# Performance work log

Hardware: AMD Instinct MI355X
Metric: run time of the kernel (lower is better)

## Reference

```python
import jax, jax.numpy as jnp
import numpy as np

N = 8192   # n_vertex
F = 1      # input_dim
H = 32     # hidden_dim
K = 2      # k_order -> hops 0..K (3 taps)
B = 2
T = 24
E = 16 * N # edges


def _sym_renorm_adj(src, dst, n):
    # A from COO ones, add self loops, D^{-1/2} (A+I) D^{-1/2}
    A = np.zeros((n, n), dtype=np.float32)
    np.add.at(A, (src, dst), 1.0)
    A += np.eye(n, dtype=np.float32)
    dinv = 1.0 / np.sqrt(A.sum(axis=1))
    return (dinv[:, None] * A * dinv[None, :]).astype(np.float32)


def setup_inputs() -> dict:
    key = jax.random.key(0)
    ks = jax.random.split(key, 16)
    rng = np.random.default_rng(0)
    src = rng.integers(0, N, size=E)
    dst = rng.integers(0, N, size=E)
    edge_index = jnp.asarray(np.stack([src, dst]).astype(np.int64))
    gso = jnp.asarray(_sym_renorm_adj(src, dst, N))
    Cin = (K + 1) * (F + H)  # stacked hop features of [x, h]
    s = 0.02
    p = lambda k, shp: (jax.random.normal(k, shp, dtype=jnp.float32) * s)
    inp = {
        "x": jax.random.normal(ks[0], (B, T, N, F), dtype=jnp.float32),
        "edge_index": edge_index,
        "gso": gso,
        "enc_Wr": p(ks[1], (Cin, H)), "enc_br": jnp.zeros((H,), jnp.float32),
        "enc_Wu": p(ks[2], (Cin, H)), "enc_bu": jnp.zeros((H,), jnp.float32),
        "enc_Wc": p(ks[3], (Cin, H)), "enc_bc": jnp.zeros((H,), jnp.float32),
        "dec_Wr": p(ks[4], (Cin, H)), "dec_br": jnp.zeros((H,), jnp.float32),
        "dec_Wu": p(ks[5], (Cin, H)), "dec_bu": jnp.zeros((H,), jnp.float32),
        "dec_Wc": p(ks[6], (Cin, H)), "dec_bc": jnp.zeros((H,), jnp.float32),
        "po_W1": p(ks[7], (H, H)), "po_b1": jnp.zeros((H,), jnp.float32),
        "po_W2": p(ks[8], (H, F)), "po_b2": jnp.zeros((F,), jnp.float32),
    }
    return inp


def _gconv(inp, gso, W, b):
    x0 = inp
    x1 = jnp.einsum("nm,bmc->bnc", gso, x0)
    x2 = jnp.einsum("nm,bmc->bnc", gso, x1)
    xs = jnp.concatenate([x0, x1, x2], axis=-1)
    return xs @ W + b


def _cell(xin, h, gso, Wr, br, Wu, bu, Wc, bc):
    # DCGRU cell: gates from K-hop graph conv of [x, h]
    xh = jnp.concatenate([xin, h], axis=-1)
    r = jax.nn.sigmoid(_gconv(xh, gso, Wr, br))
    u = jax.nn.sigmoid(_gconv(xh, gso, Wu, bu))
    c = jnp.tanh(_gconv(jnp.concatenate([xin, r * h], axis=-1), gso, Wc, bc))
    return u * h + (1.0 - u) * c


def reference(x, edge_index, gso,
              enc_Wr, enc_br, enc_Wu, enc_bu, enc_Wc, enc_bc,
              dec_Wr, dec_br, dec_Wu, dec_bu, dec_Wc, dec_bc,
              po_W1, po_b1, po_W2, po_b2):
    del edge_index  # GSO already built from it (no_grad in original)
    b, t, n, f = x.shape
    h0 = jnp.zeros((b, n, H), x.dtype)

    def enc_step(h, xt):
        return _cell(xt, h, gso, enc_Wr, enc_br, enc_Wu, enc_bu, enc_Wc, enc_bc), None

    h, _ = jax.lax.scan(enc_step, h0, jnp.transpose(x, (1, 0, 2, 3)))

    prev0 = jnp.zeros((b, n, f), x.dtype)

    def dec_step(carry, _):
        hh, prev = carry
        hh = _cell(prev, hh, gso, dec_Wr, dec_br, dec_Wu, dec_bu, dec_Wc, dec_bc)
        z = jax.nn.relu(hh @ po_W1 + po_b1)  # dropout is identity in eval
        pred = z @ po_W2 + po_b2
        return (hh, pred), pred

    _, preds = jax.lax.scan(dec_step, (h, prev0), None, length=t)
    return jnp.transpose(preds, (1, 0, 2, 3))  # (B,T,N,F)
```

## Files before the change

kernel.cpp:

```cpp
#include <hip/hip_runtime.h>


#define NV  8192
#define TT  24
#define BB  2
#define CC  33
#define JJ  66
#define HD  32
#define CAP 64
#define NPB 8

__global__ __launch_bounds__(256) void build_ell(const float* __restrict__ gso,
                                                 int* __restrict__ ellc,
                                                 float* __restrict__ ellv,
                                                 int* __restrict__ rcnt) {
    int gtid = blockIdx.x * 256 + threadIdx.x;
    int row  = gtid >> 6;
    int lane = threadIdx.x & 63;
    if (row >= NV) return;
    const float* r = gso + (size_t)row * NV;
    int cnt = 0;
    const int base = row * CAP;
    for (int c0 = 0; c0 < NV; c0 += 256) {
        const float4 v = *reinterpret_cast<const float4*>(r + c0 + lane * 4);
        const float vv[4] = {v.x, v.y, v.z, v.w};
#pragma unroll
        for (int q = 0; q < 4; ++q) {
            unsigned long long m = __ballot(vv[q] != 0.0f);
            if (vv[q] != 0.0f) {
                int pos = cnt + __popcll(m & ((1ull << lane) - 1ull));
                if (pos < CAP) {
                    ellc[base + pos] = c0 + lane * 4 + q;
                    ellv[base + pos] = vv[q];
                }
            }
            cnt += __popcll(m);
        }
    }
    if (lane == 0) rcnt[row] = cnt < CAP ? cnt : CAP;
}

__global__ __launch_bounds__(256) void init_xh(const float* __restrict__ x,
                                               float* __restrict__ XH) {
    int idx = blockIdx.x * 256 + threadIdx.x;
    if (idx >= NV * JJ) return;
    int n = idx / JJ;
    int j = idx - n * JJ;
    int b = j / CC, c = j - b * CC;
    float v = 0.f;
    if (c == 0) v = x[((size_t)b * TT + 0) * NV + n];
    XH[idx] = v;
}

__global__ __launch_bounds__(256) void spmm1(const int* __restrict__ ellc,
                                             const float* __restrict__ ellv,
                                             const int* __restrict__ rcnt,
                                             const float* __restrict__ Xin,
                                             float* __restrict__ Xout) {
    int idx = blockIdx.x * 256 + threadIdx.x;
    if (idx >= NV * 33) return;
    int n  = idx / 33;
    int j2 = idx - n * 33;
    int cnt  = rcnt[n];
    int base = n * CAP;
    float2 acc = {0.f, 0.f};
    for (int k = 0; k < cnt; ++k) {
        float s = ellv[base + k];
        const float2 xv = *reinterpret_cast<const float2*>(
            Xin + (size_t)ellc[base + k] * JJ + 2 * j2);
        acc.x = fmaf(s, xv.x, acc.x);
        acc.y = fmaf(s, xv.y, acc.y);
    }
    *reinterpret_cast<float2*>(Xout + (size_t)n * JJ + 2 * j2) = acc;
}

__global__ __launch_bounds__(256) void hop2_gates(const int* __restrict__ ellc,
                                                  const float* __restrict__ ellv,
                                                  const int* __restrict__ rcnt,
                                                  const float* __restrict__ XH,
                                                  const float* __restrict__ X1,
                                                  const float* __restrict__ Wr,
                                                  const float* __restrict__ br,
                                                  const float* __restrict__ Wu,
                                                  const float* __restrict__ bu,
                                                  float* __restrict__ U,
                                                  float* __restrict__ XC) {
    __shared__ float x2s[NPB][JJ];
    int n0 = blockIdx.x * NPB;
    for (int e = threadIdx.x; e < NPB * 33; e += 256) {
        int ln = e / 33;
        int j2 = e - ln * 33;
        int n  = n0 + ln;
        int cnt  = rcnt[n];
        int base = n * CAP;
        float2 acc = {0.f, 0.f};
        for (int k = 0; k < cnt; ++k) {
            float s = ellv[base + k];
            const float2 xv = *reinterpret_cast<const float2*>(
                X1 + (size_t)ellc[base + k] * JJ + 2 * j2);
            acc.x = fmaf(s, xv.x, acc.x);
            acc.y = fmaf(s, xv.y, acc.y);
        }
        x2s[ln][2 * j2]     = acc.x;
        x2s[ln][2 * j2 + 1] = acc.y;
    }
    __syncthreads();
    for (int e = threadIdx.x; e < NPB * BB * HD; e += 256) {
        int j  = e & 31;
        int p  = e >> 5;
        int ln = p >> 1;
        int b  = p & 1;
        int n  = n0 + ln;
        const float* xh = XH + (size_t)n * JJ + b * CC;
        const float* x1 = X1 + (size_t)n * JJ + b * CC;
        const float* x2 = &x2s[ln][b * CC];
        float accr = br[j], accu = bu[j];
#pragma unroll
        for (int i = 0; i < CC; ++i) {
            accr = fmaf(xh[i], Wr[i * HD + j], accr);
            accu = fmaf(xh[i], Wu[i * HD + j], accu);
        }
#pragma unroll
        for (int i = 0; i < CC; ++i) {
            accr = fmaf(x1[i], Wr[(CC + i) * HD + j], accr);
            accu = fmaf(x1[i], Wu[(CC + i) * HD + j], accu);
        }
#pragma unroll
        for (int i = 0; i < CC; ++i) {
            accr = fmaf(x2[i], Wr[(2 * CC + i) * HD + j], accr);
            accu = fmaf(x2[i], Wu[(2 * CC + i) * HD + j], accu);
        }
        float rg = 1.f / (1.f + expf(-accr));
        float ug = 1.f / (1.f + expf(-accu));
        U[(size_t)n * 64 + b * HD + j] = ug;
        float h = xh[1 + j];
        XC[(size_t)n * JJ + b * CC + 1 + j] = rg * h;
        if (j == 0) XC[(size_t)n * JJ + b * CC] = xh[0];
    }
}

__global__ __launch_bounds__(256) void hop2_cand(const int* __restrict__ ellc,
                                                 const float* __restrict__ ellv,
                                                 const int* __restrict__ rcnt,
                                                 const float* __restrict__ XC,
                                                 const float* __restrict__ Y1,
                                                 const float* __restrict__ Wc,
                                                 const float* __restrict__ bc,
                                                 const float* __restrict__ U,
                                                 float* __restrict__ XH,
                                                 const float* __restrict__ xsrc,
                                                 int mode, int t_next,
                                                 const float* __restrict__ W1,
                                                 const float* __restrict__ b1,
                                                 const float* __restrict__ W2,
                                                 const float* __restrict__ b2,
                                                 float* __restrict__ out,
                                                 int t_out) {
    __shared__ float y2s[NPB][JJ];
    int n0 = blockIdx.x * NPB;
    for (int e = threadIdx.x; e < NPB * 33; e += 256) {
        int ln = e / 33;
        int j2 = e - ln * 33;
        int n  = n0 + ln;
        int cnt  = rcnt[n];
        int base = n * CAP;
        float2 acc = {0.f, 0.f};
        for (int k = 0; k < cnt; ++k) {
            float s = ellv[base + k];
            const float2 xv = *reinterpret_cast<const float2*>(
                Y1 + (size_t)ellc[base + k] * JJ + 2 * j2);
            acc.x = fmaf(s, xv.x, acc.x);
            acc.y = fmaf(s, xv.y, acc.y);
        }
        y2s[ln][2 * j2]     = acc.x;
        y2s[ln][2 * j2 + 1] = acc.y;
    }
    __syncthreads();
    for (int e = threadIdx.x; e < NPB * BB * HD; e += 256) {
        int j  = e & 31;
        int p  = e >> 5;
        int ln = p >> 1;
        int b  = p & 1;
        int n  = n0 + ln;
        const float* xc = XC + (size_t)n * JJ + b * CC;
        const float* y1 = Y1 + (size_t)n * JJ + b * CC;
        const float* y2 = &y2s[ln][b * CC];
        float acc = bc[j];
#pragma unroll
        for (int i = 0; i < CC; ++i) acc = fmaf(xc[i], Wc[i * HD + j], acc);
#pragma unroll
        for (int i = 0; i < CC; ++i) acc = fmaf(y1[i], Wc[(CC + i) * HD + j], acc);
#pragma unroll
        for (int i = 0; i < CC; ++i) acc = fmaf(y2[i], Wc[(2 * CC + i) * HD + j], acc);
        float c = tanhf(acc);
        float u = U[(size_t)n * 64 + b * HD + j];
        float* hp = XH + (size_t)n * JJ + b * CC + 1 + j;
        float h = u * (*hp) + (1.f - u) * c;
        *hp = h;
        if (mode == 2) {
            float z = b1[j];
#pragma unroll
            for (int i = 0; i < HD; ++i)
                z = fmaf(__shfl(h, i, 32), W1[i * HD + j], z);
            z = fmaxf(z, 0.f);
            float pz = z * W2[j];
#pragma unroll
            for (int off = 16; off; off >>= 1) pz += __shfl_xor(pz, off, 32);
            if (j == 0) {
                float pred = pz + b2[0];
                out[((size_t)b * TT + t_out) * NV + n] = pred;
                XH[(size_t)n * JJ + b * CC] = pred;
            }
        } else if (j == 0) {
            float xin = (mode == 0) ? xsrc[((size_t)b * TT + t_next) * NV + n] : 0.f;
            XH[(size_t)n * JJ + b * CC] = xin;
        }
    }
}

extern "C" void kernel_launch(void* const* d_in, const int* in_sizes, int n_in,
                              void* d_out, int out_size, void* d_ws, size_t ws_size,
                              hipStream_t stream) {
    const float* x      = (const float*)d_in[0];
    const float* gso    = (const float*)d_in[2];
    const float* enc_Wr = (const float*)d_in[3];
    const float* enc_br = (const float*)d_in[4];
    const float* enc_Wu = (const float*)d_in[5];
    const float* enc_bu = (const float*)d_in[6];
    const float* enc_Wc = (const float*)d_in[7];
    const float* enc_bc = (const float*)d_in[8];
    const float* dec_Wr = (const float*)d_in[9];
    const float* dec_br = (const float*)d_in[10];
    const float* dec_Wu = (const float*)d_in[11];
    const float* dec_bu = (const float*)d_in[12];
    const float* dec_Wc = (const float*)d_in[13];
    const float* dec_bc = (const float*)d_in[14];
    const float* po_W1  = (const float*)d_in[15];
    const float* po_b1  = (const float*)d_in[16];
    const float* po_W2  = (const float*)d_in[17];
    const float* po_b2  = (const float*)d_in[18];
    float* out = (float*)d_out;

    char* p = (char*)d_ws;
    auto alloc = [&](size_t bytes) {
        char* q = p;
        p += (bytes + 255) & ~(size_t)255;
        return q;
    };
    int*   ellc = (int*)  alloc((size_t)NV * CAP * 4);
    float* ellv = (float*)alloc((size_t)NV * CAP * 4);
    int*   rcnt = (int*)  alloc((size_t)NV * 4);
    float* XH   = (float*)alloc((size_t)NV * JJ * 4);
    float* X1   = (float*)alloc((size_t)NV * JJ * 4);
    float* XC   = (float*)alloc((size_t)NV * JJ * 4);
    float* Y1   = (float*)alloc((size_t)NV * JJ * 4);
    float* U    = (float*)alloc((size_t)NV * 64 * 4);

    const dim3 blk(256);
    const dim3 g_build(NV / 4);
    const dim3 g_init((NV * JJ + 255) / 256);
    const dim3 g_feat2((NV * 33 + 255) / 256);
    const dim3 g_node(NV / NPB);

    hipLaunchKernelGGL(build_ell, g_build, blk, 0, stream, gso, ellc, ellv, rcnt);
    hipLaunchKernelGGL(init_xh, g_init, blk, 0, stream, x, XH);

    for (int t = 0; t < TT; ++t) {
        hipLaunchKernelGGL(spmm1, g_feat2, blk, 0, stream, ellc, ellv, rcnt, XH, X1);
        hipLaunchKernelGGL(hop2_gates, g_node, blk, 0, stream, ellc, ellv, rcnt,
                           XH, X1, enc_Wr, enc_br, enc_Wu, enc_bu, U, XC);
        hipLaunchKernelGGL(spmm1, g_feat2, blk, 0, stream, ellc, ellv, rcnt, XC, Y1);
        hipLaunchKernelGGL(hop2_cand, g_node, blk, 0, stream, ellc, ellv, rcnt,
                           XC, Y1, enc_Wc, enc_bc, U, XH,
                           x, (t + 1 < TT) ? 0 : 1, t + 1,
                           po_W1, po_b1, po_W2, po_b2, out, 0);
    }
    for (int t = 0; t < TT; ++t) {
        hipLaunchKernelGGL(spmm1, g_feat2, blk, 0, stream, ellc, ellv, rcnt, XH, X1);
        hipLaunchKernelGGL(hop2_gates, g_node, blk, 0, stream, ellc, ellv, rcnt,
                           XH, X1, dec_Wr, dec_br, dec_Wu, dec_bu, U, XC);
        hipLaunchKernelGGL(spmm1, g_feat2, blk, 0, stream, ellc, ellv, rcnt, XC, Y1);
        hipLaunchKernelGGL(hop2_cand, g_node, blk, 0, stream, ellc, ellv, rcnt,
                           XC, Y1, dec_Wc, dec_bc, U, XH,
                           x, 2, 0,
                           po_W1, po_b1, po_W2, po_b2, out, t);
    }
}
```

Baseline: 6.179 ms.

## Fuse two-hop SpMM into gate kernels via direct neighbor-of-neighbor gather

Drops the separate one-hop SpMM launches. Each gates/candidate kernel now computes both diffusion hops per node by walking neighbors of neighbors, with one 64-lane wavefront per node and shuffles for the dense weight products. The feature layout is also split into a 64-wide hidden array and a 2-wide input array, and state initialisation is folded into the ELL build. This halves launches per timestep and removes the intermediate hop-1 buffers. The price is recomputing hop-1 rows for every neighbor, which multiplies gather traffic by roughly the average degree.

```diff
diff --git a/kernel.cpp b/kernel.cpp
--- a/kernel.cpp
+++ b/kernel.cpp
@@ -3,17 +3,16 @@
 
 #define NV  8192
 #define TT  24
-#define BB  2
-#define CC  33
-#define JJ  66
+#define CAP 64
 #define HD  32
-#define CAP 64
-#define NPB 8
 
 __global__ __launch_bounds__(256) void build_ell(const float* __restrict__ gso,
                                                  int* __restrict__ ellc,
                                                  float* __restrict__ ellv,
-                                                 int* __restrict__ rcnt) {
+                                                 int* __restrict__ rcnt,
+                                                 float* __restrict__ XHh,
+                                                 float* __restrict__ XHx,
+                                                 const float* __restrict__ x) {
     int gtid = blockIdx.x * 256 + threadIdx.x;
     int row  = gtid >> 6;
     int lane = threadIdx.x & 63;
@@ -38,183 +37,131 @@
         }
     }
     if (lane == 0) rcnt[row] = cnt < CAP ? cnt : CAP;
-}
-
-__global__ __launch_bounds__(256) void init_xh(const float* __restrict__ x,
-                                               float* __restrict__ XH) {
-    int idx = blockIdx.x * 256 + threadIdx.x;
-    if (idx >= NV * JJ) return;
-    int n = idx / JJ;
-    int j = idx - n * JJ;
-    int b = j / CC, c = j - b * CC;
-    float v = 0.f;
-    if (c == 0) v = x[((size_t)b * TT + 0) * NV + n];
-    XH[idx] = v;
-}
-
-__global__ __launch_bounds__(256) void spmm1(const int* __restrict__ ellc,
-                                             const float* __restrict__ ellv,
-                                             const int* __restrict__ rcnt,
-                                             const float* __restrict__ Xin,
-                                             float* __restrict__ Xout) {
-    int idx = blockIdx.x * 256 + threadIdx.x;
-    if (idx >= NV * 33) return;
-    int n  = idx / 33;
-    int j2 = idx - n * 33;
-    int cnt  = rcnt[n];
-    int base = n * CAP;
-    float2 acc = {0.f, 0.f};
-    for (int k = 0; k < cnt; ++k) {
-        float s = ellv[base + k];
-        const float2 xv = *reinterpret_cast<const float2*>(
-            Xin + (size_t)ellc[base + k] * JJ + 2 * j2);
-        acc.x = fmaf(s, xv.x, acc.x);
-        acc.y = fmaf(s, xv.y, acc.y);
-    }
-    *reinterpret_cast<float2*>(Xout + (size_t)n * JJ + 2 * j2) = acc;
-}
-
-__global__ __launch_bounds__(256) void hop2_gates(const int* __restrict__ ellc,
-                                                  const float* __restrict__ ellv,
-                                                  const int* __restrict__ rcnt,
-                                                  const float* __restrict__ XH,
-                                                  const float* __restrict__ X1,
-                                                  const float* __restrict__ Wr,
-                                                  const float* __restrict__ br,
-                                                  const float* __restrict__ Wu,
-                                                  const float* __restrict__ bu,
-                                                  float* __restrict__ U,
-                                                  float* __restrict__ XC) {
-    __shared__ float x2s[NPB][JJ];
-    int n0 = blockIdx.x * NPB;
-    for (int e = threadIdx.x; e < NPB * 33; e += 256) {
-        int ln = e / 33;
-        int j2 = e - ln * 33;
-        int n  = n0 + ln;
-        int cnt  = rcnt[n];
-        int base = n * CAP;
-        float2 acc = {0.f, 0.f};
-        for (int k = 0; k < cnt; ++k) {
-            float s = ellv[base + k];
-            const float2 xv = *reinterpret_cast<const float2*>(
-                X1 + (size_t)ellc[base + k] * JJ + 2 * j2);
-            acc.x = fmaf(s, xv.x, acc.x);
-            acc.y = fmaf(s, xv.y, acc.y);
+    XHh[row * 64 + lane] = 0.f;
+    if (lane < 2) XHx[row * 2 + lane] = x[((size_t)lane * TT) * NV + row];
+}
+
+#define GATHER2(Fh, Fx, x1, x1x, x2, x2x)                                   \
+    float x1 = 0.f, x1x = 0.f, x2 = 0.f, x2x = 0.f;                         \
+    for (int k = 0; k < cnt; ++k) {                                         \
+        const int   ck = __shfl(myc, k);                                    \
+        const float vk = __shfl(myv, k);                                    \
+        const int   pc = __shfl(nbc, k);                                    \
+        const int   nc = lane < pc ? ellc[ck * CAP + lane] : 0;             \
+        const float nv = lane < pc ? ellv[ck * CAP + lane] : 0.f;           \
+        float a = 0.f, ax = 0.f;                                            \
+        for (int p = 0; p < pc; ++p) {                                      \
+            const int   c = __shfl(nc, p);                                  \
+            const float v = __shfl(nv, p);                                  \
+            a  = fmaf(v, Fh[c * 64 + lane], a);                             \
+            ax = fmaf(v, Fx[c * 2 + b], ax);                                \
+        }                                                                   \
+        x2 = fmaf(vk, a, x2); x2x = fmaf(vk, ax, x2x);                      \
+        if (ck == n) { x1 = a; x1x = ax; }                                  \
+    }
+
+__global__ __launch_bounds__(512) void gates_k(const int* __restrict__ ellc,
+                                               const float* __restrict__ ellv,
+                                               const int* __restrict__ rcnt,
+                                               const float* __restrict__ XHh,
+                                               const float* __restrict__ XHx,
+                                               const float* __restrict__ Wr,
+                                               const float* __restrict__ br,
+                                               const float* __restrict__ Wu,
+                                               const float* __restrict__ bu,
+                                               float* __restrict__ U,
+                                               float* __restrict__ XCh,
+                                               float* __restrict__ XCx) {
+    const int lane = threadIdx.x & 63;
+    const int j = lane & 31, b = lane >> 5, jb = b << 5;
+    const int n = blockIdx.x * 8 + (threadIdx.x >> 6);
+    const int   cnt = rcnt[n];
+    const int   myc = lane < cnt ? ellc[n * CAP + lane] : 0;
+    const float myv = lane < cnt ? ellv[n * CAP + lane] : 0.f;
+    const int   nbc = lane < cnt ? rcnt[myc] : 0;
+    GATHER2(XHh, XHx, x1, x1x, x2, x2x)
+    const float h  = XHh[n * 64 + lane];
+    const float xh = XHx[n * 2 + b];
+    float accr = br[j], accu = bu[j];
+    accr = fmaf(xh,  Wr[j],           accr);  accu = fmaf(xh,  Wu[j],           accu);
+    accr = fmaf(x1x, Wr[33 * 32 + j], accr);  accu = fmaf(x1x, Wu[33 * 32 + j], accu);
+    accr = fmaf(x2x, Wr[66 * 32 + j], accr);  accu = fmaf(x2x, Wu[66 * 32 + j], accu);
+#pragma unroll
+    for (int m = 0; m < 32; ++m) {
+        const float f0 = __shfl(h,  jb + m);
+        const float f1 = __shfl(x1, jb + m);
+        const float f2 = __shfl(x2, jb + m);
+        accr = fmaf(f0, Wr[(1 + m) * 32 + j],  accr);
+        accu = fmaf(f0, Wu[(1 + m) * 32 + j],  accu);
+        accr = fmaf(f1, Wr[(34 + m) * 32 + j], accr);
+        accu = fmaf(f1, Wu[(34 + m) * 32 + j], accu);
+        accr = fmaf(f2, Wr[(67 + m) * 32 + j], accr);
+        accu = fmaf(f2, Wu[(67 + m) * 32 + j], accu);
+    }
+    const float rg = 1.f / (1.f + expf(-accr));
+    const float ug = 1.f / (1.f + expf(-accu));
+    U[n * 64 + lane]   = ug;
+    XCh[n * 64 + lane] = rg * h;
+    if (j == 0) XCx[n * 2 + b] = xh;
+}
+
+__global__ __launch_bounds__(512) void cand_k(const int* __restrict__ ellc,
+                                              const float* __restrict__ ellv,
+                                              const int* __restrict__ rcnt,
+                                              const float* __restrict__ XCh,
+                                              const float* __restrict__ XCx,
+                                              float* XHh, float* XHx,
+                                              const float* __restrict__ U,
+                                              const float* __restrict__ Wc,
+                                              const float* __restrict__ bc,
+                                              const float* __restrict__ x,
+                                              const float* __restrict__ W1,
+                                              const float* __restrict__ b1,
+                                              const float* __restrict__ W2,
+                                              const float* __restrict__ b2,
+                                              float* __restrict__ out,
+                                              int mode, int t_next, int t_out) {
+    const int lane = threadIdx.x & 63;
+    const int j = lane & 31, b = lane >> 5, jb = b << 5;
+    const int n = blockIdx.x * 8 + (threadIdx.x >> 6);
+    const int   cnt = rcnt[n];
+    const int   myc = lane < cnt ? ellc[n * CAP + lane] : 0;
+    const float myv = lane < cnt ? ellv[n * CAP + lane] : 0.f;
+    const int   nbc = lane < cnt ? rcnt[myc] : 0;
+    GATHER2(XCh, XCx, y1, y1x, y2, y2x)
+    const float h   = XHh[n * 64 + lane];
+    const float xc  = XCx[n * 2 + b];
+    const float xch = XCh[n * 64 + lane];
+    float acc = bc[j];
+    acc = fmaf(xc,  Wc[j],           acc);
+    acc = fmaf(y1x, Wc[33 * 32 + j], acc);
+    acc = fmaf(y2x, Wc[66 * 32 + j], acc);
+#pragma unroll
+    for (int m = 0; m < 32; ++m) {
+        acc = fmaf(__shfl(xch, jb + m), Wc[(1 + m) * 32 + j],  acc);
+        acc = fmaf(__shfl(y1,  jb + m), Wc[(34 + m) * 32 + j], acc);
+        acc = fmaf(__shfl(y2,  jb + m), Wc[(67 + m) * 32 + j], acc);
+    }
+    const float cc = tanhf(acc);
+    const float u  = U[n * 64 + lane];
+    const float hn = u * h + (1.f - u) * cc;
+    XHh[n * 64 + lane] = hn;
+    if (mode == 2) {
+        float z = b1[j];
+#pragma unroll
+        for (int m = 0; m < 32; ++m)
+            z = fmaf(__shfl(hn, jb + m), W1[m * 32 + j], z);
+        float pz = fmaxf(z, 0.f) * W2[j];
+#pragma unroll
+        for (int off = 16; off; off >>= 1) pz += __shfl_xor(pz, off);
+        if (j == 0) {
+            const float pred = pz + b2[0];
+            out[((size_t)b * TT + t_out) * NV + n] = pred;
+            XHx[n * 2 + b] = pred;
         }
-        x2s[ln][2 * j2]     = acc.x;
-        x2s[ln][2 * j2 + 1] = acc.y;
-    }
-    __syncthreads();
-    for (int e = threadIdx.x; e < NPB * BB * HD; e += 256) {
-        int j  = e & 31;
-        int p  = e >> 5;
-        int ln = p >> 1;
-        int b  = p & 1;
-        int n  = n0 + ln;
-        const float* xh = XH + (size_t)n * JJ + b * CC;
-        const float* x1 = X1 + (size_t)n * JJ + b * CC;
-        const float* x2 = &x2s[ln][b * CC];
-        float accr = br[j], accu = bu[j];
-#pragma unroll
-        for (int i = 0; i < CC; ++i) {
-            accr = fmaf(xh[i], Wr[i * HD + j], accr);
-            accu = fmaf(xh[i], Wu[i * HD + j], accu);
-        }
-#pragma unroll
-        for (int i = 0; i < CC; ++i) {
-            accr = fmaf(x1[i], Wr[(CC + i) * HD + j], accr);
-            accu = fmaf(x1[i], Wu[(CC + i) * HD + j], accu);
-        }
-#pragma unroll
-        for (int i = 0; i < CC; ++i) {
-            accr = fmaf(x2[i], Wr[(2 * CC + i) * HD + j], accr);
-            accu = fmaf(x2[i], Wu[(2 * CC + i) * HD + j], accu);
-        }
-        float rg = 1.f / (1.f + expf(-accr));
-        float ug = 1.f / (1.f + expf(-accu));
-        U[(size_t)n * 64 + b * HD + j] = ug;
-        float h = xh[1 + j];
-        XC[(size_t)n * JJ + b * CC + 1 + j] = rg * h;
-        if (j == 0) XC[(size_t)n * JJ + b * CC] = xh[0];
-    }
-}
-
-__global__ __launch_bounds__(256) void hop2_cand(const int* __restrict__ ellc,
-                                                 const float* __restrict__ ellv,
-                                                 const int* __restrict__ rcnt,
-                                                 const float* __restrict__ XC,
-                                                 const float* __restrict__ Y1,
-                                                 const float* __restrict__ Wc,
-                                                 const float* __restrict__ bc,
-                                                 const float* __restrict__ U,
-                                                 float* __restrict__ XH,
-                                                 const float* __restrict__ xsrc,
-                                                 int mode, int t_next,
-                                                 const float* __restrict__ W1,
-                                                 const float* __restrict__ b1,
-                                                 const float* __restrict__ W2,
-                                                 const float* __restrict__ b2,
-                                                 float* __restrict__ out,
-                                                 int t_out) {
-    __shared__ float y2s[NPB][JJ];
-    int n0 = blockIdx.x * NPB;
-    for (int e = threadIdx.x; e < NPB * 33; e += 256) {
-        int ln = e / 33;
-        int j2 = e - ln * 33;
-        int n  = n0 + ln;
-        int cnt  = rcnt[n];
-        int base = n * CAP;
-        float2 acc = {0.f, 0.f};
-        for (int k = 0; k < cnt; ++k) {
-            float s = ellv[base + k];
-            const float2 xv = *reinterpret_cast<const float2*>(
-                Y1 + (size_t)ellc[base + k] * JJ + 2 * j2);
-            acc.x = fmaf(s, xv.x, acc.x);
-            acc.y = fmaf(s, xv.y, acc.y);
-        }
-        y2s[ln][2 * j2]     = acc.x;
-        y2s[ln][2 * j2 + 1] = acc.y;
-    }
-    __syncthreads();
-    for (int e = threadIdx.x; e < NPB * BB * HD; e += 256) {
-        int j  = e & 31;
-        int p  = e >> 5;
-        int ln = p >> 1;
-        int b  = p & 1;
-        int n  = n0 + ln;
-        const float* xc = XC + (size_t)n * JJ + b * CC;
-        const float* y1 = Y1 + (size_t)n * JJ + b * CC;
-        const float* y2 = &y2s[ln][b * CC];
-        float acc = bc[j];
-#pragma unroll
-        for (int i = 0; i < CC; ++i) acc = fmaf(xc[i], Wc[i * HD + j], acc);
-#pragma unroll
-        for (int i = 0; i < CC; ++i) acc = fmaf(y1[i], Wc[(CC + i) * HD + j], acc);
-#pragma unroll
-        for (int i = 0; i < CC; ++i) acc = fmaf(y2[i], Wc[(2 * CC + i) * HD + j], acc);
-        float c = tanhf(acc);
-        float u = U[(size_t)n * 64 + b * HD + j];
-        float* hp = XH + (size_t)n * JJ + b * CC + 1 + j;
-        float h = u * (*hp) + (1.f - u) * c;
-        *hp = h;
-        if (mode == 2) {
-            float z = b1[j];
-#pragma unroll
-            for (int i = 0; i < HD; ++i)
-                z = fmaf(__shfl(h, i, 32), W1[i * HD + j], z);
-            z = fmaxf(z, 0.f);
-            float pz = z * W2[j];
-#pragma unroll
-            for (int off = 16; off; off >>= 1) pz += __shfl_xor(pz, off, 32);
-            if (j == 0) {
-                float pred = pz + b2[0];
-                out[((size_t)b * TT + t_out) * NV + n] = pred;
-                XH[(size_t)n * JJ + b * CC] = pred;
-            }
-        } else if (j == 0) {
-            float xin = (mode == 0) ? xsrc[((size_t)b * TT + t_next) * NV + n] : 0.f;
-            XH[(size_t)n * JJ + b * CC] = xin;
-        }
+    } else if (j == 0) {
+        XHx[n * 2 + b] = (mode == 0)
+            ? x[((size_t)b * TT + t_next) * NV + n] : 0.f;
     }
 }
 
@@ -250,39 +197,34 @@
     int*   ellc = (int*)  alloc((size_t)NV * CAP * 4);
     float* ellv = (float*)alloc((size_t)NV * CAP * 4);
     int*   rcnt = (int*)  alloc((size_t)NV * 4);
-    float* XH   = (float*)alloc((size_t)NV * JJ * 4);
-    float* X1   = (float*)alloc((size_t)NV * JJ * 4);
-    float* XC   = (float*)alloc((size_t)NV * JJ * 4);
-    float* Y1   = (float*)alloc((size_t)NV * JJ * 4);
+    float* XHh  = (float*)alloc((size_t)NV * 64 * 4);
+    float* XHx  = (float*)alloc((size_t)NV * 2 * 4);
+    float* XCh  = (float*)alloc((size_t)NV * 64 * 4);
+    float* XCx  = (float*)alloc((size_t)NV * 2 * 4);
     float* U    = (float*)alloc((size_t)NV * 64 * 4);
 
-    const dim3 blk(256);
-    const dim3 g_build(NV / 4);
-    const dim3 g_init((NV * JJ + 255) / 256);
-    const dim3 g_feat2((NV * 33 + 255) / 256);
-    const dim3 g_node(NV / NPB);
-
-    hipLaunchKernelGGL(build_ell, g_build, blk, 0, stream, gso, ellc, ellv, rcnt);
-    hipLaunchKernelGGL(init_xh, g_init, blk, 0, stream, x, XH);
+    const dim3 blk(512);
+    const dim3 g_node(NV / 8);
+
+    hipLaunchKernelGGL(build_ell, dim3(NV / 4), dim3(256), 0, stream,
+                       gso, ellc, ellv, rcnt, XHh, XHx, x);
 
     for (int t = 0; t < TT; ++t) {
-        hipLaunchKernelGGL(spmm1, g_feat2, blk, 0, stream, ellc, ellv, rcnt, XH, X1);
-        hipLaunchKernelGGL(hop2_gates, g_node, blk, 0, stream, ellc, ellv, rcnt,
-                           XH, X1, enc_Wr, enc_br, enc_Wu, enc_bu, U, XC);
-        hipLaunchKernelGGL(spmm1, g_feat2, blk, 0, stream, ellc, ellv, rcnt, XC, Y1);
-        hipLaunchKernelGGL(hop2_cand, g_node, blk, 0, stream, ellc, ellv, rcnt,
-                           XC, Y1, enc_Wc, enc_bc, U, XH,
-                           x, (t + 1 < TT) ? 0 : 1, t + 1,
-                           po_W1, po_b1, po_W2, po_b2, out, 0);
+        hipLaunchKernelGGL(gates_k, g_node, blk, 0, stream,
+                           ellc, ellv, rcnt, XHh, XHx,
+                           enc_Wr, enc_br, enc_Wu, enc_bu, U, XCh, XCx);
+        hipLaunchKernelGGL(cand_k, g_node, blk, 0, stream,
+                           ellc, ellv, rcnt, XCh, XCx, XHh, XHx, U,
+                           enc_Wc, enc_bc, x, po_W1, po_b1, po_W2, po_b2,
+                           out, (t + 1 < TT) ? 0 : 1, t + 1, 0);
     }
     for (int t = 0; t < TT; ++t) {
-        hipLaunchKernelGGL(spmm1, g_feat2, blk, 0, stream, ellc, ellv, rcnt, XH, X1);
-        hipLaunchKernelGGL(hop2_gates, g_node, blk, 0, stream, ellc, ellv, rcnt,
-                           XH, X1, dec_Wr, dec_br, dec_Wu, dec_bu, U, XC);
-        hipLaunchKernelGGL(spmm1, g_feat2, blk, 0, stream, ellc, ellv, rcnt, XC, Y1);
-        hipLaunchKernelGGL(hop2_cand, g_node, blk, 0, stream, ellc, ellv, rcnt,
-                           XC, Y1, dec_Wc, dec_bc, U, XH,
-                           x, 2, 0,
-                           po_W1, po_b1, po_W2, po_b2, out, t);
-    }
-}
+        hipLaunchKernelGGL(gates_k, g_node, blk, 0, stream,
+                           ellc, ellv, rcnt, XHh, XHx,
+                           dec_Wr, dec_br, dec_Wu, dec_bu, U, XCh, XCx);
+        hipLaunchKernelGGL(cand_k, g_node, blk, 0, stream,
+                           ellc, ellv, rcnt, XCh, XCx, XHh, XHx, U,
+                           dec_Wc, dec_bc, x, po_W1, po_b1, po_W2, po_b2,
+                           out, 2, 0, t);
+    }
+}
```

After: 12.97 ms. +109.9%, slower.
